# Optimization experiments

Hardware: AMD Instinct MI355X
Metric: run time of the kernel (lower is better)

## Reference

```python
import jax, jax.numpy as jnp
import numpy as np

NUM_LABELS = 5  # background + 4 lane instances; all present w.h.p. given 2M random pixels


def setup_inputs() -> dict:
    key = jax.random.key(0)
    k1, k2 = jax.random.split(key)
    prediction = jax.random.normal(k1, (1, 4, 1024, 2048), dtype=jnp.float32)
    correct_label = jax.random.randint(k2, (1, 1024, 2048), 0, NUM_LABELS, dtype=jnp.int64)
    delta_v = jnp.float32(0.5)
    delta_d = jnp.float32(3.0)
    return {"prediction": prediction, "correct_label": correct_label,
            "delta_v": delta_v, "delta_d": delta_d}


def _safe_norm(sq):
    # sqrt with zero-safe gradient (matches torch.norm value; avoids NaN in vjp)
    nz = sq > 0
    return jnp.where(nz, jnp.sqrt(jnp.where(nz, sq, 1.0)), 0.0)


def _loss(prediction, correct_label, delta_v, delta_d):
    K = NUM_LABELS
    N, C, H, W = prediction.shape  # N == 1 (module only valid for batch 1)
    pred = prediction.reshape(C, H * W)          # [C, HW]
    lab = correct_label.reshape(H * W)           # [HW]; labels 0..K-1 => unique inverse == labels

    # scatter-mean centroids (torch_scatter 'mean' clamps empty counts to 1 -> mean 0)
    counts = jax.ops.segment_sum(jnp.ones((H * W,), pred.dtype), lab, num_segments=K)  # [K]
    sums = jax.ops.segment_sum(pred.T, lab, num_segments=K)                            # [K, C]
    muc = sums / jnp.maximum(counts, 1.0)[:, None]                                     # [K, C]

    # L_var: pull pixels toward their instance centroid
    diff = muc[lab] - pred.T                     # [HW, C] gather of centroids
    dsq = jnp.sum(diff * diff, axis=1)           # [HW]
    hinge = jnp.maximum(_safe_norm(dsq) - delta_v, 0.0)
    var = hinge * hinge                          # [HW]
    L_var_per = jax.ops.segment_sum(var, lab, num_segments=K) / jnp.maximum(counts, 1.0)
    L_var = jnp.sum(L_var_per) / K

    # L_dist: push distinct centroids apart (vectorized over A != B pairs)
    cdiff = muc[:, None, :] - muc[None, :, :]    # [K, K, C]
    csq = jnp.sum(cdiff * cdiff, axis=-1)        # [K, K]
    cd = _safe_norm(csq)
    offdiag = 1.0 - jnp.eye(K, dtype=pred.dtype)
    dh = jnp.maximum(delta_d - cd, 0.0)
    L_dist = jnp.sum(dh * dh * offdiag) / (K * (K - 1))

    return L_var + L_dist


def reference(prediction, correct_label, delta_v, delta_d):
    return _loss(prediction, correct_label, delta_v, delta_d)
```

## Files before the change

### kernel.cpp

```cpp
#include <hip/hip_runtime.h>


constexpr int K   = 5;
constexpr int C   = 4;
constexpr int NB  = 1024;
constexpr int TPB = 256;
constexpr int PPT = 8;
constexpr int RED_TPB = 1024;

__device__ __forceinline__ float wave_reduce_sum(float v) {
#pragma unroll
  for (int off = 32; off > 0; off >>= 1) v += __shfl_down(v, off, 64);
  return v;
}

__device__ __forceinline__ float wave_col_sum(const float* __restrict__ colp, int lane) {
  const float4* p4 = reinterpret_cast<const float4*>(colp);
  float4 a0 = p4[lane];
  float4 a1 = p4[lane + 64];
  float4 a2 = p4[lane + 128];
  float4 a3 = p4[lane + 192];
  float s = (a0.x + a0.y) + (a0.z + a0.w);
  s += (a1.x + a1.y) + (a1.z + a1.w);
  s += (a2.x + a2.y) + (a2.z + a2.w);
  s += (a3.x + a3.y) + (a3.z + a3.w);
  return wave_reduce_sum(s);
}

__global__ __launch_bounds__(TPB) void k_stats(
    const float* __restrict__ pred, const int* __restrict__ lab,
    float* __restrict__ partial, int HW) {
  const int tid = threadIdx.x;

  float cnt[K] = {0.f, 0.f, 0.f, 0.f, 0.f};
  float sum[K][C] = {};

  const long long chunk_stride = (long long)NB * TPB * PPT;
  for (long long chunk = (long long)blockIdx.x * TPB * PPT; chunk < HW;
       chunk += chunk_stride) {
    const long long p0 = chunk + (long long)tid * PPT;
    if (p0 + PPT <= HW) {
      int4 la = *reinterpret_cast<const int4*>(lab + p0);
      int4 lb = *reinterpret_cast<const int4*>(lab + p0 + 4);
      int labv[PPT] = {la.x, la.y, la.z, la.w, lb.x, lb.y, lb.z, lb.w};
      float x[PPT][C];
#pragma unroll
      for (int c = 0; c < C; ++c) {
        const float* base = pred + (long long)c * HW + p0;
        float4 a = *reinterpret_cast<const float4*>(base);
        float4 b = *reinterpret_cast<const float4*>(base + 4);
        x[0][c] = a.x; x[1][c] = a.y; x[2][c] = a.z; x[3][c] = a.w;
        x[4][c] = b.x; x[5][c] = b.y; x[6][c] = b.z; x[7][c] = b.w;
      }
#pragma unroll
      for (int p = 0; p < PPT; ++p) {
        const int l = labv[p];
#pragma unroll
        for (int k = 0; k < K; ++k) {
          const float m = (l == k) ? 1.0f : 0.0f;
          cnt[k] += m;
#pragma unroll
          for (int c = 0; c < C; ++c) sum[k][c] = fmaf(m, x[p][c], sum[k][c]);
        }
      }
    } else if (p0 < HW) {
      for (int p = 0; p < PPT && p0 + p < HW; ++p) {
        const int l = lab[p0 + p];
        for (int k = 0; k < K; ++k) {
          const float m = (l == k) ? 1.0f : 0.0f;
          cnt[k] += m;
          for (int c = 0; c < C; ++c)
            sum[k][c] = fmaf(m, pred[(long long)c * HW + p0 + p], sum[k][c]);
        }
      }
    }
  }

  __shared__ float red[TPB / 64][25];
  const int wave = tid >> 6, lane = tid & 63;
#pragma unroll
  for (int j = 0; j < 25; ++j) {
    float v = (j < K) ? cnt[j] : sum[(j - K) >> 2][(j - K) & 3];
    v = wave_reduce_sum(v);
    if (lane == 0) red[wave][j] = v;
  }
  __syncthreads();
  if (tid < 25) {
    float t = red[0][tid] + red[1][tid] + red[2][tid] + red[3][tid];
    partial[tid * NB + blockIdx.x] = t;
  }
}

__global__ __launch_bounds__(RED_TPB) void k_centroids(
    const float* __restrict__ partial, const float* __restrict__ dd_p,
    float* __restrict__ finals) {
  __shared__ float tot[25];
  const int tid = threadIdx.x, wave = tid >> 6, lane = tid & 63;
  for (int col = wave; col < 25; col += RED_TPB / 64) {
    float v = wave_col_sum(partial + col * NB, lane);
    if (lane == 0) tot[col] = v;
  }
  __syncthreads();
  if (tid == 0) {
    const float dd = dd_p[0];
    float cnt[K], mu[K][C];
#pragma unroll
    for (int k = 0; k < K; ++k) {
      cnt[k] = tot[k];
      const float inv = 1.0f / fmaxf(cnt[k], 1.0f);
#pragma unroll
      for (int c = 0; c < C; ++c) mu[k][c] = tot[K + k * C + c] * inv;
    }
    float ld = 0.f;
#pragma unroll
    for (int a = 0; a < K; ++a) {
#pragma unroll
      for (int b = 0; b < K; ++b) {
        if (a == b) continue;
        float csq = 0.f;
#pragma unroll
        for (int c = 0; c < C; ++c) {
          const float d = mu[a][c] - mu[b][c];
          csq = fmaf(d, d, csq);
        }
        const float cd = csq > 0.f ? sqrtf(csq) : 0.f;
        const float dh = fmaxf(dd - cd, 0.f);
        ld = fmaf(dh, dh, ld);
      }
    }
    ld *= 1.0f / (float)(K * (K - 1));
#pragma unroll
    for (int k = 0; k < K; ++k) finals[k] = cnt[k];
#pragma unroll
    for (int k = 0; k < K; ++k)
#pragma unroll
      for (int c = 0; c < C; ++c) finals[K + k * C + c] = mu[k][c];
    finals[25] = ld;
  }
}

__global__ __launch_bounds__(TPB) void k_var(
    const float* __restrict__ pred, const int* __restrict__ lab,
    const float* __restrict__ finals, const float* __restrict__ dv_p,
    float* __restrict__ vpartial, int HW) {
  __shared__ __align__(16) float smu[K * C];
  if (threadIdx.x < K * C) smu[threadIdx.x] = finals[K + threadIdx.x];
  __syncthreads();
  const float dv = dv_p[0];
  const int tid = threadIdx.x;

  float vs[K] = {};

  const long long chunk_stride = (long long)NB * TPB * PPT;
  for (long long chunk = (long long)blockIdx.x * TPB * PPT; chunk < HW;
       chunk += chunk_stride) {
    const long long p0 = chunk + (long long)tid * PPT;
    if (p0 + PPT <= HW) {
      int4 la = *reinterpret_cast<const int4*>(lab + p0);
      int4 lb = *reinterpret_cast<const int4*>(lab + p0 + 4);
      int labv[PPT] = {la.x, la.y, la.z, la.w, lb.x, lb.y, lb.z, lb.w};
      float x[PPT][C];
#pragma unroll
      for (int c = 0; c < C; ++c) {
        const float* base = pred + (long long)c * HW + p0;
        float4 a = *reinterpret_cast<const float4*>(base);
        float4 b = *reinterpret_cast<const float4*>(base + 4);
        x[0][c] = a.x; x[1][c] = a.y; x[2][c] = a.z; x[3][c] = a.w;
        x[4][c] = b.x; x[5][c] = b.y; x[6][c] = b.z; x[7][c] = b.w;
      }
#pragma unroll
      for (int p = 0; p < PPT; ++p) {
        const int l = labv[p];
        const float4 mu = *reinterpret_cast<const float4*>(&smu[l * C]);
        const float d0 = mu.x - x[p][0];
        const float d1 = mu.y - x[p][1];
        const float d2 = mu.z - x[p][2];
        const float d3 = mu.w - x[p][3];
        float dsq = d0 * d0;
        dsq = fmaf(d1, d1, dsq);
        dsq = fmaf(d2, d2, dsq);
        dsq = fmaf(d3, d3, dsq);
        const float dn = dsq > 0.f ? sqrtf(dsq) : 0.f;
        const float h  = fmaxf(dn - dv, 0.f);
        const float var = h * h;
#pragma unroll
        for (int k = 0; k < K; ++k) vs[k] += (l == k) ? var : 0.f;
      }
    } else if (p0 < HW) {
      for (int p = 0; p < PPT && p0 + p < HW; ++p) {
        const int l = lab[p0 + p];
        float dsq = 0.f;
        for (int c = 0; c < C; ++c) {
          const float d = smu[l * C + c] - pred[(long long)c * HW + p0 + p];
          dsq = fmaf(d, d, dsq);
        }
        const float dn = dsq > 0.f ? sqrtf(dsq) : 0.f;
        const float h  = fmaxf(dn - dv, 0.f);
        const float var = h * h;
        for (int k = 0; k < K; ++k) vs[k] += (l == k) ? var : 0.f;
      }
    }
  }

  __shared__ float red[TPB / 64][K];
  const int wave = tid >> 6, lane = tid & 63;
#pragma unroll
  for (int j = 0; j < K; ++j) {
    float v = wave_reduce_sum(vs[j]);
    if (lane == 0) red[wave][j] = v;
  }
  __syncthreads();
  if (tid < K) {
    float t = red[0][tid] + red[1][tid] + red[2][tid] + red[3][tid];
    vpartial[tid * NB + blockIdx.x] = t;
  }
}

__global__ __launch_bounds__(RED_TPB) void k_final(
    const float* __restrict__ vpartial, const float* __restrict__ finals,
    float* __restrict__ out) {
  __shared__ float tot[K];
  const int tid = threadIdx.x, wave = tid >> 6, lane = tid & 63;
  if (wave < K) {
    float v = wave_col_sum(vpartial + wave * NB, lane);
    if (lane == 0) tot[wave] = v;
  }
  __syncthreads();
  if (tid == 0) {
    float lvar = 0.f;
#pragma unroll
    for (int k = 0; k < K; ++k) lvar += tot[k] / fmaxf(finals[k], 1.0f);
    lvar *= 1.0f / (float)K;
    out[0] = lvar + finals[25];
  }
}

extern "C" void kernel_launch(void* const* d_in, const int* in_sizes, int n_in,
                              void* d_out, int out_size, void* d_ws, size_t ws_size,
                              hipStream_t stream) {
  const float* pred = (const float*)d_in[0];
  const int*   lab  = (const int*)d_in[1];
  const float* dv   = (const float*)d_in[2];
  const float* dd   = (const float*)d_in[3];
  float*       out  = (float*)d_out;

  const int HW = in_sizes[1];

  float* ws     = (float*)d_ws;
  float* part1  = ws;
  float* finals = ws + 25 * NB;
  float* vpart  = ws + 25 * NB + 32;

  k_stats    <<<NB, TPB, 0, stream>>>(pred, lab, part1, HW);
  k_centroids<<<1,  RED_TPB, 0, stream>>>(part1, dd, finals);
  k_var      <<<NB, TPB, 0, stream>>>(pred, lab, finals, dv, vpart, HW);
  k_final    <<<1,  RED_TPB, 0, stream>>>(vpart, finals, out);
}
```

Before: 33.26 us.

## Fuse four-kernel pipeline into one cooperative kernel with grid-wide flag barrier

```diff
diff --git a/kernel.cpp b/kernel.cpp
--- a/kernel.cpp
+++ b/kernel.cpp
@@ -3,10 +3,11 @@
 
 constexpr int K   = 5;
 constexpr int C   = 4;
-constexpr int NB  = 1024;
 constexpr int TPB = 256;
 constexpr int PPT = 8;
-constexpr int RED_TPB = 1024;
+constexpr int NB  = 1024;
+constexpr int NGROUP  = 32;
+constexpr int GSTRIDE = 16;
 
 __device__ __forceinline__ float wave_reduce_sum(float v) {
 #pragma unroll
@@ -14,27 +15,230 @@
   return v;
 }
 
-__device__ __forceinline__ float wave_col_sum(const float* __restrict__ colp, int lane) {
+__device__ __forceinline__ float wave_col_sum(const float* __restrict__ colp,
+                                              int lane, int nb) {
   const float4* p4 = reinterpret_cast<const float4*>(colp);
-  float4 a0 = p4[lane];
-  float4 a1 = p4[lane + 64];
-  float4 a2 = p4[lane + 128];
-  float4 a3 = p4[lane + 192];
-  float s = (a0.x + a0.y) + (a0.z + a0.w);
-  s += (a1.x + a1.y) + (a1.z + a1.w);
-  s += (a2.x + a2.y) + (a2.z + a2.w);
-  s += (a3.x + a3.y) + (a3.z + a3.w);
+  float s = 0.f;
+  for (int r = lane; r < (nb >> 2); r += 64) {
+    float4 a = p4[r];
+    s += (a.x + a.y) + (a.z + a.w);
+  }
   return wave_reduce_sum(s);
 }
+
+__device__ __forceinline__ bool hier_arrive_last(int* __restrict__ gtick,
+                                                 int* __restrict__ stick,
+                                                 int bid, int nb) {
+  const int g = atomicAdd(&gtick[(bid & (NGROUP - 1)) * GSTRIDE], 1);
+  if (g == nb / NGROUP - 1) {
+    return atomicAdd(stick, 1) == NGROUP - 1;
+  }
+  return false;
+}
+
+__global__ __launch_bounds__(TPB, 4) void k_fused(
+    const float* __restrict__ pred, const int* __restrict__ lab,
+    const float* __restrict__ dv_p, const float* __restrict__ dd_p,
+    float* __restrict__ partial, float* __restrict__ finals,
+    float* __restrict__ vpart, int* __restrict__ bar,
+    float* __restrict__ out, int HW) {
+  const int tid = threadIdx.x, bid = blockIdx.x;
+  const int wave = tid >> 6, lane = tid & 63;
+  const int nb = gridDim.x;
+
+  int* gtick1 = bar;
+  int* stick1 = bar + NGROUP * GSTRIDE;
+  int* flag1  = bar + NGROUP * GSTRIDE + 16;
+  int* gtick2 = bar + NGROUP * GSTRIDE + 32;
+  int* stick2 = bar + 2 * NGROUP * GSTRIDE + 32;
+
+  const long long p0 = ((long long)bid * TPB + tid) * PPT;
+  float x[PPT][C];
+  int labv[PPT];
+  if (p0 + PPT <= HW) {
+    int4 la = *reinterpret_cast<const int4*>(lab + p0);
+    int4 lb = *reinterpret_cast<const int4*>(lab + p0 + 4);
+    labv[0]=la.x; labv[1]=la.y; labv[2]=la.z; labv[3]=la.w;
+    labv[4]=lb.x; labv[5]=lb.y; labv[6]=lb.z; labv[7]=lb.w;
+#pragma unroll
+    for (int c = 0; c < C; ++c) {
+      const float* base = pred + (long long)c * HW + p0;
+      float4 a = *reinterpret_cast<const float4*>(base);
+      float4 b = *reinterpret_cast<const float4*>(base + 4);
+      x[0][c]=a.x; x[1][c]=a.y; x[2][c]=a.z; x[3][c]=a.w;
+      x[4][c]=b.x; x[5][c]=b.y; x[6][c]=b.z; x[7][c]=b.w;
+    }
+  } else {
+#pragma unroll
+    for (int p = 0; p < PPT; ++p) {
+      if (p0 + p < HW) {
+        labv[p] = lab[p0 + p];
+#pragma unroll
+        for (int c = 0; c < C; ++c) x[p][c] = pred[(long long)c * HW + p0 + p];
+      } else {
+        labv[p] = -1;
+#pragma unroll
+        for (int c = 0; c < C; ++c) x[p][c] = 0.f;
+      }
+    }
+  }
+
+  float cnt[K] = {0.f, 0.f, 0.f, 0.f, 0.f};
+  float sum[K][C] = {};
+#pragma unroll
+  for (int p = 0; p < PPT; ++p) {
+    const int l = labv[p];
+#pragma unroll
+    for (int k = 0; k < K; ++k) {
+      const float m = (l == k) ? 1.0f : 0.0f;
+      cnt[k] += m;
+#pragma unroll
+      for (int c = 0; c < C; ++c) sum[k][c] = fmaf(m, x[p][c], sum[k][c]);
+    }
+  }
+
+  __shared__ float red[TPB / 64][25];
+#pragma unroll
+  for (int j = 0; j < 25; ++j) {
+    float v = (j < K) ? cnt[j] : sum[(j - K) >> 2][(j - K) & 3];
+    v = wave_reduce_sum(v);
+    if (lane == 0) red[wave][j] = v;
+  }
+  __syncthreads();
+  if (tid < 25) {
+    float t = red[0][tid] + red[1][tid] + red[2][tid] + red[3][tid];
+    atomicExch(&partial[tid * nb + bid], t);
+  }
+  __syncthreads();
+
+  __shared__ int lastA;
+  if (tid == 0) lastA = hier_arrive_last(gtick1, stick1, bid, nb) ? 1 : 0;
+  __syncthreads();
+  if (lastA) {
+    __threadfence();
+    __shared__ float tot[25];
+    for (int col = wave; col < 25; col += TPB / 64) {
+      float v = wave_col_sum(partial + col * nb, lane, nb);
+      if (lane == 0) tot[col] = v;
+    }
+    __syncthreads();
+    if (tid == 0) {
+      const float dd = dd_p[0];
+      float cntv[K], mu[K][C];
+#pragma unroll
+      for (int k = 0; k < K; ++k) {
+        cntv[k] = tot[k];
+        const float inv = 1.0f / fmaxf(cntv[k], 1.0f);
+#pragma unroll
+        for (int c = 0; c < C; ++c) mu[k][c] = tot[K + k * C + c] * inv;
+      }
+      float ld = 0.f;
+#pragma unroll
+      for (int a = 0; a < K; ++a) {
+#pragma unroll
+        for (int b = 0; b < K; ++b) {
+          if (a == b) continue;
+          float csq = 0.f;
+#pragma unroll
+          for (int c = 0; c < C; ++c) {
+            const float d = mu[a][c] - mu[b][c];
+            csq = fmaf(d, d, csq);
+          }
+          const float cd = csq > 0.f ? sqrtf(csq) : 0.f;
+          const float dh = fmaxf(dd - cd, 0.f);
+          ld = fmaf(dh, dh, ld);
+        }
+      }
+      ld *= 1.0f / (float)(K * (K - 1));
+#pragma unroll
+      for (int k = 0; k < K; ++k) atomicExch(&finals[k], cntv[k]);
+#pragma unroll
+      for (int k = 0; k < K; ++k)
+#pragma unroll
+        for (int c = 0; c < C; ++c) atomicExch(&finals[K + k * C + c], mu[k][c]);
+      atomicExch(&finals[25], ld);
+      __threadfence();
+      atomicExch(flag1, 1);
+    }
+  }
+
+  if (tid == 0) {
+    while (__hip_atomic_load(flag1, __ATOMIC_RELAXED,
+                             __HIP_MEMORY_SCOPE_AGENT) == 0)
+      __builtin_amdgcn_s_sleep(2);
+  }
+  __syncthreads();
+
+  __shared__ float smu[K * C];
+  if (tid < K * C)
+    smu[tid] = __hip_atomic_load(&finals[K + tid], __ATOMIC_RELAXED,
+                                 __HIP_MEMORY_SCOPE_AGENT);
+  __syncthreads();
+  const float dv = dv_p[0];
+
+  float vs[K] = {};
+#pragma unroll
+  for (int p = 0; p < PPT; ++p) {
+    const int l = labv[p];
+    if (l >= 0) {
+      const float d0 = smu[l * C + 0] - x[p][0];
+      const float d1 = smu[l * C + 1] - x[p][1];
+      const float d2 = smu[l * C + 2] - x[p][2];
+      const float d3 = smu[l * C + 3] - x[p][3];
+      float dsq = d0 * d0;
+      dsq = fmaf(d1, d1, dsq);
+      dsq = fmaf(d2, d2, dsq);
+      dsq = fmaf(d3, d3, dsq);
+      const float dn = dsq > 0.f ? sqrtf(dsq) : 0.f;
+      const float h  = fmaxf(dn - dv, 0.f);
+      const float var = h * h;
+#pragma unroll
+      for (int k = 0; k < K; ++k) vs[k] += (l == k) ? var : 0.f;
+    }
+  }
+
+  __shared__ float red2[TPB / 64][K];
+#pragma unroll
+  for (int j = 0; j < K; ++j) {
+    float v = wave_reduce_sum(vs[j]);
+    if (lane == 0) red2[wave][j] = v;
+  }
+  __syncthreads();
+  if (tid < K) {
+    float t = red2[0][tid] + red2[1][tid] + red2[2][tid] + red2[3][tid];
+    atomicExch(&vpart[tid * nb + bid], t);
+  }
+  __syncthreads();
+
+  __shared__ int lastB;
+  if (tid == 0) lastB = hier_arrive_last(gtick2, stick2, bid, nb) ? 1 : 0;
+  __syncthreads();
+  if (!lastB) return;
+
+  __threadfence();
+  __shared__ float tot2[K];
+  for (int col = wave; col < K; col += TPB / 64) {
+    float v = wave_col_sum(vpart + col * nb, lane, nb);
+    if (lane == 0) tot2[col] = v;
+  }
+  __syncthreads();
+  if (tid == 0) {
+    float lvar = 0.f;
+#pragma unroll
+    for (int k = 0; k < K; ++k) lvar += tot2[k] / fmaxf(finals[k], 1.0f);
+    lvar *= 1.0f / (float)K;
+    out[0] = lvar + finals[25];
+  }
+}
+
+constexpr int RED_TPB = 1024;
 
 __global__ __launch_bounds__(TPB) void k_stats(
     const float* __restrict__ pred, const int* __restrict__ lab,
     float* __restrict__ partial, int HW) {
   const int tid = threadIdx.x;
-
   float cnt[K] = {0.f, 0.f, 0.f, 0.f, 0.f};
   float sum[K][C] = {};
-
   const long long chunk_stride = (long long)NB * TPB * PPT;
   for (long long chunk = (long long)blockIdx.x * TPB * PPT; chunk < HW;
        chunk += chunk_stride) {
@@ -49,8 +253,8 @@
         const float* base = pred + (long long)c * HW + p0;
         float4 a = *reinterpret_cast<const float4*>(base);
         float4 b = *reinterpret_cast<const float4*>(base + 4);
-        x[0][c] = a.x; x[1][c] = a.y; x[2][c] = a.z; x[3][c] = a.w;
-        x[4][c] = b.x; x[5][c] = b.y; x[6][c] = b.z; x[7][c] = b.w;
+        x[0][c]=a.x; x[1][c]=a.y; x[2][c]=a.z; x[3][c]=a.w;
+        x[4][c]=b.x; x[5][c]=b.y; x[6][c]=b.z; x[7][c]=b.w;
       }
 #pragma unroll
       for (int p = 0; p < PPT; ++p) {
@@ -75,7 +279,6 @@
       }
     }
   }
-
   __shared__ float red[TPB / 64][25];
   const int wave = tid >> 6, lane = tid & 63;
 #pragma unroll
@@ -97,7 +300,7 @@
   __shared__ float tot[25];
   const int tid = threadIdx.x, wave = tid >> 6, lane = tid & 63;
   for (int col = wave; col < 25; col += RED_TPB / 64) {
-    float v = wave_col_sum(partial + col * NB, lane);
+    float v = wave_col_sum(partial + col * NB, lane, NB);
     if (lane == 0) tot[col] = v;
   }
   __syncthreads();
@@ -113,7 +316,7 @@
     }
     float ld = 0.f;
 #pragma unroll
-    for (int a = 0; a < K; ++a) {
+    for (int a = 0; a < K; ++a)
 #pragma unroll
       for (int b = 0; b < K; ++b) {
         if (a == b) continue;
@@ -127,7 +330,6 @@
         const float dh = fmaxf(dd - cd, 0.f);
         ld = fmaf(dh, dh, ld);
       }
-    }
     ld *= 1.0f / (float)(K * (K - 1));
 #pragma unroll
     for (int k = 0; k < K; ++k) finals[k] = cnt[k];
@@ -148,9 +350,7 @@
   __syncthreads();
   const float dv = dv_p[0];
   const int tid = threadIdx.x;
-
   float vs[K] = {};
-
   const long long chunk_stride = (long long)NB * TPB * PPT;
   for (long long chunk = (long long)blockIdx.x * TPB * PPT; chunk < HW;
        chunk += chunk_stride) {
@@ -165,8 +365,8 @@
         const float* base = pred + (long long)c * HW + p0;
         float4 a = *reinterpret_cast<const float4*>(base);
         float4 b = *reinterpret_cast<const float4*>(base + 4);
-        x[0][c] = a.x; x[1][c] = a.y; x[2][c] = a.z; x[3][c] = a.w;
-        x[4][c] = b.x; x[5][c] = b.y; x[6][c] = b.z; x[7][c] = b.w;
+        x[0][c]=a.x; x[1][c]=a.y; x[2][c]=a.z; x[3][c]=a.w;
+        x[4][c]=b.x; x[5][c]=b.y; x[6][c]=b.z; x[7][c]=b.w;
       }
 #pragma unroll
       for (int p = 0; p < PPT; ++p) {
@@ -201,7 +401,6 @@
       }
     }
   }
-
   __shared__ float red[TPB / 64][K];
   const int wave = tid >> 6, lane = tid & 63;
 #pragma unroll
@@ -222,7 +421,7 @@
   __shared__ float tot[K];
   const int tid = threadIdx.x, wave = tid >> 6, lane = tid & 63;
   if (wave < K) {
-    float v = wave_col_sum(vpartial + wave * NB, lane);
+    float v = wave_col_sum(vpartial + wave * NB, lane, NB);
     if (lane == 0) tot[wave] = v;
   }
   __syncthreads();
@@ -250,9 +449,21 @@
   float* part1  = ws;
   float* finals = ws + 25 * NB;
   float* vpart  = ws + 25 * NB + 32;
-
-  k_stats    <<<NB, TPB, 0, stream>>>(pred, lab, part1, HW);
-  k_centroids<<<1,  RED_TPB, 0, stream>>>(part1, dd, finals);
-  k_var      <<<NB, TPB, 0, stream>>>(pred, lab, finals, dv, vpart, HW);
-  k_final    <<<1,  RED_TPB, 0, stream>>>(vpart, finals, out);
-}
+  int*   bar    = (int*)(ws + 25 * NB + 32 + K * NB);
+  const int bar_ints = 2 * NGROUP * GSTRIDE + 64;
+
+  hipMemsetAsync(bar, 0, bar_ints * sizeof(int), stream);
+
+  void* args[] = {(void*)&pred, (void*)&lab, (void*)&dv, (void*)&dd,
+                  (void*)&part1, (void*)&finals, (void*)&vpart,
+                  (void*)&bar, (void*)&out, (void*)&HW};
+  hipError_t err = hipLaunchCooperativeKernel(
+      (const void*)k_fused, dim3(NB), dim3(TPB), args, 0, stream);
+
+  if (err != hipSuccess) {
+    k_stats    <<<NB, TPB, 0, stream>>>(pred, lab, part1, HW);
+    k_centroids<<<1,  RED_TPB, 0, stream>>>(part1, dd, finals);
+    k_var      <<<NB, TPB, 0, stream>>>(pred, lab, finals, dv, vpart, HW);
+    k_final    <<<1,  RED_TPB, 0, stream>>>(vpart, finals, out);
+  }
+}
```

After: 64.69 us. 94.5% more time.
